# Optimization experiments

Hardware: AMD Instinct MI355X
Metric: run time of the kernel (lower is better)

Reference implementation:

```python
import jax, jax.numpy as jnp
import numpy as np

B, S, HID = 1, 2048, 4096
NH, NKV, D = 32, 8, 128
SCALE = D ** -0.5


def _rope_tables(seq_len, head_dim, base=10000.0):
    inv_freq = 1.0 / (base ** (jnp.arange(0, head_dim, 2, dtype=jnp.float32) / head_dim))
    freqs = jnp.arange(seq_len, dtype=jnp.float32)[:, None] * inv_freq[None, :]  # [S, D/2]
    emb = jnp.concatenate([freqs, freqs], axis=-1)  # [S, D]
    return jnp.cos(emb), jnp.sin(emb)


def _rotate_half(x):
    half = x.shape[-1] // 2
    return jnp.concatenate([-x[..., half:], x[..., :half]], axis=-1)


def setup_inputs() -> dict:
    key = jax.random.key(0)
    ks = jax.random.split(key, 5)
    hidden = jax.random.normal(ks[0], (B, S, HID), dtype=jnp.float32)
    cos, sin = _rope_tables(S, D)
    # additive causal mask: 0 on/below diagonal, large negative above
    neg = jnp.full((S, S), -1e9, dtype=jnp.float32)
    causal_mask = jnp.triu(neg, k=1)[None, None]  # [1,1,S,S]
    std_in = HID ** -0.5
    Wq = jax.random.normal(ks[1], (HID, NH * D), dtype=jnp.float32) * std_in
    Wk = jax.random.normal(ks[2], (HID, NKV * D), dtype=jnp.float32) * std_in
    Wv = jax.random.normal(ks[3], (HID, NKV * D), dtype=jnp.float32) * std_in
    Wo = jax.random.normal(ks[4], (NH * D, HID), dtype=jnp.float32) * ((NH * D) ** -0.5)
    return {"hidden": hidden, "cos": cos, "sin": sin, "causal_mask": causal_mask,
            "Wq": Wq, "Wk": Wk, "Wv": Wv, "Wo": Wo}


def reference(hidden, cos, sin, causal_mask, Wq, Wk, Wv, Wo):
    b, s, _ = hidden.shape
    q = (hidden @ Wq).reshape(b, s, NH, D).transpose(0, 2, 1, 3)    # [B,H,S,D]
    k = (hidden @ Wk).reshape(b, s, NKV, D).transpose(0, 2, 1, 3)   # [B,Hkv,S,D]
    v = (hidden @ Wv).reshape(b, s, NKV, D).transpose(0, 2, 1, 3)
    c = cos[None, None]  # [1,1,S,D]
    sn = sin[None, None]
    q = q * c + _rotate_half(q) * sn
    k = k * c + _rotate_half(k) * sn
    group = NH // NKV
    if group > 1:
        k = jnp.repeat(k, group, axis=1)  # [B,H,S,D]
        v = jnp.repeat(v, group, axis=1)
    scores = jnp.einsum('bhsd,bhtd->bhst', q, k) * SCALE + causal_mask
    attn = jax.nn.softmax(scores.astype(jnp.float32), axis=-1).astype(v.dtype)
    ctx = jnp.einsum('bhst,bhtd->bhsd', attn, v)
    ctx = ctx.transpose(0, 2, 1, 3).reshape(b, s, NH * D)
    return ctx @ Wo
```

## Files before the change

### kernel.cpp

```cpp
#include <hip/hip_runtime.h>
#include <hip/hip_bf16.h>
#include <cstdint>
#include <cstddef>

typedef __attribute__((ext_vector_type(8))) short bf16x8;
typedef __attribute__((ext_vector_type(4))) float f32x4;
typedef __attribute__((ext_vector_type(16))) float f32x16;
typedef __attribute__((ext_vector_type(4))) unsigned int u32x4;

__device__ __forceinline__ unsigned short f2bf(float f) {
  __hip_bfloat16 h = __float2bfloat16(f);
  return *reinterpret_cast<unsigned short*>(&h);
}
__device__ __forceinline__ float bf2f(unsigned short u) {
  __hip_bfloat16 h = *reinterpret_cast<__hip_bfloat16*>(&u);
  return __bfloat162float(h);
}

typedef const __attribute__((address_space(1))) void gas_void;
typedef __attribute__((address_space(3))) void las_void;
__device__ __forceinline__ void gload_lds16(const void* g, void* l) {
  __builtin_amdgcn_global_load_lds((gas_void*)g, (las_void*)l, 16, 0, 0);
}

template <int N>
__device__ __forceinline__ void waitcnt_vm() {
  asm volatile("s_waitcnt vmcnt(%0)" :: "i"(N) : "memory");
}

#define S_LEN 2048
#define HID 4096
#define NH 32
#define NKV 8
#define HD 128
#define NQKV 6144
static const float ATT_SCALE = 0.08838834764831845f;


__global__ void prep_kernel(const float* __restrict__ hidden, short* __restrict__ hid_bf,
                            const float* __restrict__ Wq, const float* __restrict__ Wk,
                            const float* __restrict__ Wv, const float* __restrict__ Wo,
                            short* __restrict__ Wcat, short* __restrict__ WoT) {
  __shared__ float tile[64][33];
  const int bid = blockIdx.x;
  const int t = threadIdx.x;
  if (bid >= 20480) {
    int i = ((bid - 20480) * 256 + t) * 8;
    f32x4 a = *(const f32x4*)(hidden + i);
    f32x4 b = *(const f32x4*)(hidden + i + 4);
    unsigned short o[8];
#pragma unroll
    for (int k = 0; k < 4; ++k) { o[k] = f2bf(a[k]); o[4 + k] = f2bf(b[k]); }
    *(u32x4*)(hid_bf + i) = *(const u32x4*)o;
    return;
  }
  const float* src; short* dst; int N, loc;
  if (bid < 8192)       { src = Wq; dst = Wcat;                      N = 4096; loc = bid; }
  else if (bid < 10240) { src = Wk; dst = Wcat + (size_t)4096 * HID; N = 1024; loc = bid - 8192; }
  else if (bid < 12288) { src = Wv; dst = Wcat + (size_t)5120 * HID; N = 1024; loc = bid - 10240; }
  else                  { src = Wo; dst = WoT;                       N = 4096; loc = bid - 12288; }
  const int kb = (loc & 63) * 64, nb = (loc >> 6) * 32;
  {
    int kr = t >> 3, c4 = (t & 7) * 4;
#pragma unroll
    for (int i = 0; i < 2; ++i) {
      int k = kr + i * 32;
      f32x4 v = *(const f32x4*)(src + (size_t)(kb + k) * N + nb + c4);
      tile[k][c4] = v[0]; tile[k][c4 + 1] = v[1];
      tile[k][c4 + 2] = v[2]; tile[k][c4 + 3] = v[3];
    }
  }
  __syncthreads();
  int n = t >> 3, k0 = (t & 7) * 8;
  unsigned short o[8];
#pragma unroll
  for (int i = 0; i < 8; ++i) o[i] = f2bf(tile[k0 + i][n]);
  *(u32x4*)(dst + (size_t)(nb + n) * HID + kb + k0) = *(const u32x4*)o;
}


template <int MODE, int BM, int BN, int WM, int WN>
__global__ __launch_bounds__(WM * WN * 64, 2) void gemm32_kernel(
    const short* __restrict__ A, const short* __restrict__ Bt,
    int M, int N, int K,
    float* __restrict__ Cf, short* __restrict__ qb_,
    short* __restrict__ kb_, short* __restrict__ vb_) {
  constexpr int NT = WM * WN * 64;
  constexpr int MT = BM / (WM * 32);
  constexpr int NTL = BN / (WN * 32);
  constexpr int LA = (BM / 2) * 8 / NT;
  constexpr int LB = (BN / 2) * 8 / NT;
  constexpr int BUF = (BM + BN) * 64;

  __shared__ short lds[2 * BUF];

  const int tid = threadIdx.x, wid = tid >> 6, lane = tid & 63;
  const int wr = wid / WN, wc = wid % WN;
  const int l31 = lane & 31, lh = lane >> 5;
  const int brow = blockIdx.y * BM, bcol = blockIdx.x * BN;
  const int T = K >> 6;

  f32x16 acc[MT][NTL] = {};

  auto stage_rgn = [&](int kt, int rgn) {
    short* buf = lds + (kt & 1) * BUF;
    if (rgn == 0 || rgn == 3) {
      const int mh = (rgn == 3);
      short* dst = buf + mh * (BM / 2) * 64;
      const short* src = A + (size_t)(brow + mh * (BM / 2)) * K + kt * 64;
#pragma unroll
      for (int i = 0; i < LA; ++i) {
        int slot = i * NT + tid;
        int row = slot >> 3, c2 = slot & 7;
        gload_lds16(src + (size_t)row * K + ((c2 ^ (row & 7)) * 8), dst + slot * 8);
      }
    } else {
      const int nh = (rgn == 2);
      short* dst = buf + BM * 64 + nh * (BN / 2) * 64;
      const short* src = Bt + (size_t)(bcol + nh * (BN / 2)) * K + kt * 64;
#pragma unroll
      for (int i = 0; i < LB; ++i) {
        int slot = i * NT + tid;
        int row = slot >> 3, c2 = slot & 7;
        gload_lds16(src + (size_t)row * K + ((c2 ^ (row & 7)) * 8), dst + slot * 8);
      }
    }
  };

  stage_rgn(0, 0); stage_rgn(0, 1); stage_rgn(0, 2); stage_rgn(0, 3);

  for (int kt = 0; kt < T; ++kt) {
    const bool nl = (kt + 1 < T);
    waitcnt_vm<0>();
    __builtin_amdgcn_s_barrier();
    __builtin_amdgcn_sched_barrier(0);
    if (nl) { stage_rgn(kt + 1, 0); stage_rgn(kt + 1, 1);
              stage_rgn(kt + 1, 2); stage_rgn(kt + 1, 3); }

    const short* As_ = lds + (kt & 1) * BUF;
    const short* Bs_ = As_ + BM * 64;
#pragma unroll
    for (int st = 0; st < 4; ++st) {
      bf16x8 af[MT], bf[NTL];
      const int c = st * 2 + lh;
#pragma unroll
      for (int mt = 0; mt < MT; ++mt) {
        int row = wr * (BM / WM) + mt * 32 + l31;
        af[mt] = *(const bf16x8*)(As_ + row * 64 + ((c ^ (row & 7)) * 8));
      }
#pragma unroll
      for (int nt = 0; nt < NTL; ++nt) {
        int row = wc * (BN / WN) + nt * 32 + l31;
        bf[nt] = *(const bf16x8*)(Bs_ + row * 64 + ((c ^ (row & 7)) * 8));
      }
      __builtin_amdgcn_s_setprio(1);
#pragma unroll
      for (int mt = 0; mt < MT; ++mt)
#pragma unroll
        for (int nt = 0; nt < NTL; ++nt)
          acc[mt][nt] = __builtin_amdgcn_mfma_f32_32x32x16_bf16(
              af[mt], bf[nt], acc[mt][nt], 0, 0, 0);
      __builtin_amdgcn_s_setprio(0);
    }
  }

  if (MODE == 0) {
#pragma unroll
    for (int mt = 0; mt < MT; ++mt)
#pragma unroll
      for (int nt = 0; nt < NTL; ++nt)
#pragma unroll
        for (int reg = 0; reg < 16; ++reg) {
          int row = brow + wr * (BM / WM) + mt * 32 + (reg & 3) + 8 * (reg >> 2) + 4 * lh;
          int col = bcol + wc * (BN / WN) + nt * 32 + l31;
          Cf[(size_t)row * N + col] = acc[mt][nt][reg];
        }
  } else {
#pragma unroll
    for (int nt = 0; nt < NTL; ++nt) {
      const int cb = bcol + wc * (BN / WN) + nt * 32;
      const int d = (cb & 127) + l31;
      if (cb < 4096) {
        unsigned short* dst = (unsigned short*)qb_ + (size_t)(cb >> 7) * S_LEN * HD;
#pragma unroll
        for (int mt = 0; mt < MT; ++mt)
#pragma unroll
          for (int reg = 0; reg < 16; ++reg) {
            int row = brow + wr * (BM / WM) + mt * 32 + (reg & 3) + 8 * (reg >> 2) + 4 * lh;
            dst[(size_t)row * HD + d] = f2bf(acc[mt][nt][reg]);
          }
      } else if (cb < 5120) {
        char* base = (char*)kb_ + ((size_t)((cb - 4096) >> 7) << 19);
#pragma unroll
        for (int mt = 0; mt < MT; ++mt)
#pragma unroll
          for (int reg = 0; reg < 16; ++reg) {
            int row = brow + wr * (BM / WM) + mt * 32 + (reg & 3) + 8 * (reg >> 2) + 4 * lh;
            int krow = row & 63;
            size_t off = ((size_t)(row >> 6) << 14) +
                         ((((krow << 8) + ((d >> 3) << 4)) ^ ((krow & 7) << 4)) + ((d & 7) << 1));
            *(unsigned short*)(base + off) = f2bf(acc[mt][nt][reg]);
          }
      } else {
        char* base = (char*)vb_ + ((size_t)((cb - 5120) >> 7) << 19);
#pragma unroll
        for (int mt = 0; mt < MT; ++mt)
#pragma unroll
          for (int reg = 0; reg < 16; ++reg) {
            int row = brow + wr * (BM / WM) + mt * 32 + (reg & 3) + 8 * (reg >> 2) + 4 * lh;
            int sl = row & 63;
            size_t off = ((size_t)(row >> 6) << 14) +
                         ((((d << 7) + ((sl >> 3) << 4)) ^ ((d & 7) << 4)) + ((sl & 7) << 1));
            *(unsigned short*)(base + off) = f2bf(acc[mt][nt][reg]);
          }
      }
    }
  }
}

__global__ void rope_kernel(short* __restrict__ qbuf, short* __restrict__ kbuf,
                            const float* __restrict__ cosT, const float* __restrict__ sinT) {
  int idx = blockIdx.x * 256 + threadIdx.x;
  const int total = (NH + NKV) * S_LEN * 64;
  if (idx >= total) return;
  int d = idx & 63;
  int rowi = idx >> 6;
  int s;
  unsigned short *p1, *p2;
  if (rowi < NH * S_LEN) {
    unsigned short* base = (unsigned short*)qbuf + (size_t)rowi * HD;
    s = rowi & (S_LEN - 1);
    p1 = base + d; p2 = base + d + 64;
  } else {
    int kr = rowi - NH * S_LEN;
    int kvh = kr >> 11; s = kr & (S_LEN - 1);
    char* base = (char*)kbuf + ((size_t)kvh << 19) + ((size_t)(s >> 6) << 14);
    int krow = s & 63, swz = (krow & 7) << 4;
    int dd = d + 64;
    p1 = (unsigned short*)(base + ((((krow << 8) + ((d >> 3) << 4)) ^ swz) + ((d & 7) << 1)));
    p2 = (unsigned short*)(base + ((((krow << 8) + ((dd >> 3) << 4)) ^ swz) + ((dd & 7) << 1)));
  }
  float x1 = bf2f(*p1);
  float x2 = bf2f(*p2);
  float c1 = cosT[s * HD + d], s1 = sinT[s * HD + d];
  *p1 = f2bf(x1 * c1 - x2 * s1);
  *p2 = f2bf(x2 * c1 + x1 * s1);
}

__global__ __launch_bounds__(512, 2) void attn_kernel(const short* __restrict__ qb_,
                                                      const short* __restrict__ kb_,
                                                      const short* __restrict__ vb_,
                                                      short* __restrict__ ctx) {
  const int bid = blockIdx.x;
  const int kvh = bid & 7;
  const int idx = bid >> 3;
  const int h = kvh * 4 + (idx & 3);
  const int slot = idx >> 2;
  const int tid = threadIdx.x, wid = tid >> 6, lane = tid & 63;
  const int r = lane & 15, g = lane >> 4;

  __shared__ short Ks[2][64 * 128];
  __shared__ short Vts[2][128 * 64];
  __shared__ short Ps[8][16 * 64];

  const int qb2s[2] = { slot, 15 - slot };
  const int nt0 = 2 * qb2s[0] + 2;
  const int T = 34;

  const char* kvbase_k = (const char*)kb_ + ((size_t)kvh << 19);
  const char* kvbase_v = (const char*)vb_ + ((size_t)kvh << 19);

  auto stage = [&](int tg, int b) {
    int kvt = (tg < nt0) ? tg : (tg - nt0);
    const char* kt = kvbase_k + ((size_t)kvt << 14);
    const char* vt = kvbase_v + ((size_t)kvt << 14);
#pragma unroll
    for (int i = 0; i < 2; ++i) {
      int ch = i * 8 + wid;
      gload_lds16(kt + ch * 1024 + lane * 16, (char*)&Ks[b][0] + ch * 1024);
      gload_lds16(vt + ch * 1024 + lane * 16, (char*)&Vts[b][0] + ch * 1024);
    }
  };

  stage(0, 0);
  int cur = 0, tglob = 0;

  for (int sec = 0; sec < 2; ++sec) {
    const int qb2 = qb2s[sec];
    const int nt = 2 * qb2 + 2;
    const int rowbase = qb2 * 128 + wid * 16;

    const unsigned short* qptr =
        (const unsigned short*)qb_ + ((size_t)h * S_LEN + rowbase) * HD;
    bf16x8 qf[4];
#pragma unroll
    for (int s4 = 0; s4 < 4; ++s4)
      qf[s4] = *(const bf16x8*)(qptr + (size_t)r * HD + s4 * 32 + g * 8);

    f32x4 oacc[8] = {};
    float m_run[4], l_run[4];
#pragma unroll
    for (int j = 0; j < 4; ++j) { m_run[j] = -1e30f; l_run[j] = 0.f; }

    for (int kvt = 0; kvt < nt; ++kvt, ++tglob) {
      __syncthreads();
      if (tglob + 1 < T) stage(tglob + 1, cur ^ 1);

      const char* Kc = (const char*)&Ks[cur][0];
      const char* Vc = (const char*)&Vts[cur][0];

      f32x4 sv[4] = {};
      __builtin_amdgcn_s_setprio(1);
#pragma unroll
      for (int n = 0; n < 4; ++n) {
        int krow = n * 16 + r;
        int swz = (krow & 7) << 4;
#pragma unroll
        for (int s4 = 0; s4 < 4; ++s4) {
          bf16x8 kf = *(const bf16x8*)(Kc + ((krow * 256 + s4 * 64 + g * 16) ^ swz));
          sv[n] = __builtin_amdgcn_mfma_f32_16x16x32_bf16(qf[s4], kf, sv[n], 0, 0, 0);
        }
      }
      __builtin_amdgcn_s_setprio(0);

      if (kvt * 64 + 63 > rowbase) {
#pragma unroll
        for (int n = 0; n < 4; ++n)
#pragma unroll
          for (int j = 0; j < 4; ++j) {
            int colg = kvt * 64 + n * 16 + r;
            int rowg = rowbase + g * 4 + j;
            sv[n][j] = (colg <= rowg) ? sv[n][j] * ATT_SCALE : -1e30f;
          }
      } else {
#pragma unroll
        for (int n = 0; n < 4; ++n)
#pragma unroll
          for (int j = 0; j < 4; ++j) sv[n][j] *= ATT_SCALE;
      }

      float pmax[4];
#pragma unroll
      for (int j = 0; j < 4; ++j)
        pmax[j] = fmaxf(fmaxf(sv[0][j], sv[1][j]), fmaxf(sv[2][j], sv[3][j]));
#pragma unroll
      for (int msk = 1; msk <= 8; msk <<= 1)
#pragma unroll
        for (int j = 0; j < 4; ++j) pmax[j] = fmaxf(pmax[j], __shfl_xor(pmax[j], msk));

      float sf[4], rsum[4];
#pragma unroll
      for (int j = 0; j < 4; ++j) {
        float mn = fmaxf(m_run[j], pmax[j]);
        sf[j] = __expf(m_run[j] - mn);
        m_run[j] = mn;
        rsum[j] = 0.f;
      }
#pragma unroll
      for (int n = 0; n < 4; ++n)
#pragma unroll
        for (int j = 0; j < 4; ++j) {
          float p = __expf(sv[n][j] - m_run[j]);
          sv[n][j] = p;
          rsum[j] += p;
        }
#pragma unroll
      for (int msk = 1; msk <= 8; msk <<= 1)
#pragma unroll
        for (int j = 0; j < 4; ++j) rsum[j] += __shfl_xor(rsum[j], msk);
#pragma unroll
      for (int j = 0; j < 4; ++j) l_run[j] = l_run[j] * sf[j] + rsum[j];
#pragma unroll
      for (int t = 0; t < 8; ++t)
#pragma unroll
        for (int j = 0; j < 4; ++j) oacc[t][j] *= sf[j];

#pragma unroll
      for (int n = 0; n < 4; ++n)
#pragma unroll
        for (int j = 0; j < 4; ++j) {
          int prow = g * 4 + j, pcol = n * 16 + r;
          int poff = (prow * 128 + pcol * 2) ^ ((prow & 7) << 4);
          *(unsigned short*)((char*)&Ps[wid][0] + poff) = f2bf(sv[n][j]);
        }

      __builtin_amdgcn_s_setprio(1);
#pragma unroll
      for (int s4 = 0; s4 < 2; ++s4) {
        bf16x8 pf = *(const bf16x8*)((const char*)&Ps[wid][0] +
                                     ((r * 128 + s4 * 64 + g * 16) ^ ((r & 7) << 4)));
#pragma unroll
        for (int t = 0; t < 8; ++t) {
          int vrow = t * 16 + r;
          bf16x8 vf = *(const bf16x8*)(Vc + ((vrow * 128 + s4 * 64 + g * 16) ^ ((vrow & 7) << 4)));
          oacc[t] = __builtin_amdgcn_mfma_f32_16x16x32_bf16(pf, vf, oacc[t], 0, 0, 0);
        }
      }
      __builtin_amdgcn_s_setprio(0);
      cur ^= 1;
    }

    float inv[4];
#pragma unroll
    for (int j = 0; j < 4; ++j) inv[j] = 1.0f / l_run[j];
#pragma unroll
    for (int t = 0; t < 8; ++t)
#pragma unroll
      for (int j = 0; j < 4; ++j) {
        int rowg = rowbase + g * 4 + j;
        int colg = h * HD + t * 16 + r;
        ((unsigned short*)ctx)[(size_t)rowg * HID + colg] = f2bf(oacc[t][j] * inv[j]);
      }
  }
}

extern "C" void kernel_launch(void* const* d_in, const int* in_sizes, int n_in,
                              void* d_out, int out_size, void* d_ws, size_t ws_size,
                              hipStream_t stream) {
  const float* hidden = (const float*)d_in[0];
  const float* cosT   = (const float*)d_in[1];
  const float* sinT   = (const float*)d_in[2];
  const float* Wq = (const float*)d_in[4];
  const float* Wk = (const float*)d_in[5];
  const float* Wv = (const float*)d_in[6];
  const float* Wo = (const float*)d_in[7];
  float* out = (float*)d_out;

  char* ws = (char*)d_ws;
  short* hid_bf = (short*)(ws);
  short* Wcat   = (short*)(ws + 16777216);
  short* WoT    = (short*)(ws + 67108864);
  short* qbuf   = (short*)(ws + 100663296);
  short* kbuf   = (short*)(ws + 117440512);
  short* vbuf   = (short*)(ws + 121634816);
  short* ctx    = (short*)(ws + 125829120);

  prep_kernel<<<24576, 256, 0, stream>>>(hidden, hid_bf, Wq, Wk, Wv, Wo, Wcat, WoT);

  gemm32_kernel<1, 128, 384, 2, 4><<<dim3(16, 16), 512, 0, stream>>>(
      hid_bf, Wcat, S_LEN, NQKV, HID, nullptr, qbuf, kbuf, vbuf);

  rope_kernel<<<20480, 256, 0, stream>>>(qbuf, kbuf, cosT, sinT);

  attn_kernel<<<256, 512, 0, stream>>>(qbuf, kbuf, vbuf, ctx);

  gemm32_kernel<0, 128, 256, 2, 4><<<dim3(16, 16), 512, 0, stream>>>(
      ctx, WoT, S_LEN, HID, HID, out, nullptr, nullptr, nullptr);
}
```

Baseline: 338.8 us.

## Pre-tile GEMM operands into contiguous block layout for linear LDS staging

The prep kernel and the attention epilogue now write hidden, the concatenated QKV weights, Wo^T and ctx in a tiled layout. Each 64-wide k-slice of a 128-row (or BN-row) block becomes one contiguous chunk, grouped by 8-element column. The GEMM then stages each tile with fully linear 16-byte global-to-LDS loads and reads fragments without XOR swizzle arithmetic. This is meant to make the global loads perfectly coalesced and cut address math. The trade-offs are that the hidden conversion becomes a transpose through shared memory, ctx is written with scattered 2-byte stores, and the LDS reads lose their bank-conflict swizzle.

Result: faster. 327.5 us (-3.3%).

```diff
diff --git a/kernel.cpp b/kernel.cpp
--- a/kernel.cpp
+++ b/kernel.cpp
@@ -44,21 +44,35 @@
   __shared__ float tile[64][33];
   const int bid = blockIdx.x;
   const int t = threadIdx.x;
+
   if (bid >= 20480) {
-    int i = ((bid - 20480) * 256 + t) * 8;
-    f32x4 a = *(const f32x4*)(hidden + i);
-    f32x4 b = *(const f32x4*)(hidden + i + 4);
+    const int hbid = bid - 20480;
+    const int kb = (hbid & 63) * 64, sb = (hbid >> 6) * 32;
+    {
+      int sr = t >> 3, k4 = (t & 7) * 4;
+#pragma unroll
+      for (int i = 0; i < 2; ++i) {
+        f32x4 v = *(const f32x4*)(hidden + (size_t)(sb + sr) * HID + kb + i * 32 + k4);
+#pragma unroll
+        for (int jj = 0; jj < 4; ++jj) tile[i * 32 + k4 + jj][sr] = v[jj];
+      }
+    }
+    __syncthreads();
+    const int ts = t & 31, c = t >> 5;
+    const int s = sb + ts;
     unsigned short o[8];
 #pragma unroll
-    for (int k = 0; k < 4; ++k) { o[k] = f2bf(a[k]); o[4 + k] = f2bf(b[k]); }
-    *(u32x4*)(hid_bf + i) = *(const u32x4*)o;
+    for (int i = 0; i < 8; ++i) o[i] = f2bf(tile[c * 8 + i][ts]);
+    size_t off16 = (((size_t)(s >> 7) * 64 + (kb >> 6)) * 8 + c) * 128 + (s & 127);
+    *(u32x4*)(hid_bf + off16 * 8) = *(const u32x4*)o;
     return;
   }
-  const float* src; short* dst; int N, loc;
-  if (bid < 8192)       { src = Wq; dst = Wcat;                      N = 4096; loc = bid; }
-  else if (bid < 10240) { src = Wk; dst = Wcat + (size_t)4096 * HID; N = 1024; loc = bid - 8192; }
-  else if (bid < 12288) { src = Wv; dst = Wcat + (size_t)5120 * HID; N = 1024; loc = bid - 10240; }
-  else                  { src = Wo; dst = WoT;                       N = 4096; loc = bid - 12288; }
+
+  const float* src; short* dst; int N, loc, noff, BNp;
+  if (bid < 8192)       { src = Wq; dst = Wcat; N = 4096; loc = bid;         noff = 0;    BNp = 384; }
+  else if (bid < 10240) { src = Wk; dst = Wcat; N = 1024; loc = bid - 8192;  noff = 4096; BNp = 384; }
+  else if (bid < 12288) { src = Wv; dst = Wcat; N = 1024; loc = bid - 10240; noff = 5120; BNp = 384; }
+  else                  { src = Wo; dst = WoT;  N = 4096; loc = bid - 12288; noff = 0;    BNp = 256; }
   const int kb = (loc & 63) * 64, nb = (loc >> 6) * 32;
   {
     int kr = t >> 3, c4 = (t & 7) * 4;
@@ -71,26 +85,30 @@
     }
   }
   __syncthreads();
-  int n = t >> 3, k0 = (t & 7) * 8;
+  const int tn = t & 31, c = t >> 5;
+  const int n = noff + nb + tn;
+  const int nblk = n / BNp, nrow = n % BNp;
   unsigned short o[8];
 #pragma unroll
-  for (int i = 0; i < 8; ++i) o[i] = f2bf(tile[k0 + i][n]);
-  *(u32x4*)(dst + (size_t)(nb + n) * HID + kb + k0) = *(const u32x4*)o;
-}
-
-
-template <int MODE, int BM, int BN, int WM, int WN>
-__global__ __launch_bounds__(WM * WN * 64, 2) void gemm32_kernel(
+  for (int i = 0; i < 8; ++i) o[i] = f2bf(tile[c * 8 + i][tn]);
+  size_t off16 = (((size_t)nblk * 64 + (kb >> 6)) * 8 + c) * BNp + nrow;
+  *(u32x4*)(dst + off16 * 8) = *(const u32x4*)o;
+}
+
+template <int MODE, int BN>
+__global__ __launch_bounds__(512, 2) void gemm32t_kernel(
     const short* __restrict__ A, const short* __restrict__ Bt,
-    int M, int N, int K,
+    int N, int K,
     float* __restrict__ Cf, short* __restrict__ qb_,
     short* __restrict__ kb_, short* __restrict__ vb_) {
-  constexpr int NT = WM * WN * 64;
+  constexpr int BM = 128, WM = 2, WN = 4;
   constexpr int MT = BM / (WM * 32);
   constexpr int NTL = BN / (WN * 32);
-  constexpr int LA = (BM / 2) * 8 / NT;
-  constexpr int LB = (BN / 2) * 8 / NT;
-  constexpr int BUF = (BM + BN) * 64;
+  constexpr int ASZ = 8 * BM * 8;
+  constexpr int BSZ = 8 * BN * 8;
+  constexpr int LA = ASZ / (512 * 8);
+  constexpr int LB = BSZ / (512 * 8);
+  constexpr int BUF = ASZ + BSZ;
 
   __shared__ short lds[2 * BUF];
 
@@ -102,57 +120,44 @@
 
   f32x16 acc[MT][NTL] = {};
 
-  auto stage_rgn = [&](int kt, int rgn) {
-    short* buf = lds + (kt & 1) * BUF;
-    if (rgn == 0 || rgn == 3) {
-      const int mh = (rgn == 3);
-      short* dst = buf + mh * (BM / 2) * 64;
-      const short* src = A + (size_t)(brow + mh * (BM / 2)) * K + kt * 64;
-#pragma unroll
-      for (int i = 0; i < LA; ++i) {
-        int slot = i * NT + tid;
-        int row = slot >> 3, c2 = slot & 7;
-        gload_lds16(src + (size_t)row * K + ((c2 ^ (row & 7)) * 8), dst + slot * 8);
-      }
-    } else {
-      const int nh = (rgn == 2);
-      short* dst = buf + BM * 64 + nh * (BN / 2) * 64;
-      const short* src = Bt + (size_t)(bcol + nh * (BN / 2)) * K + kt * 64;
-#pragma unroll
-      for (int i = 0; i < LB; ++i) {
-        int slot = i * NT + tid;
-        int row = slot >> 3, c2 = slot & 7;
-        gload_lds16(src + (size_t)row * K + ((c2 ^ (row & 7)) * 8), dst + slot * 8);
-      }
+  auto stage = [&](int kt) {
+    short* dstA = lds + (kt & 1) * BUF;
+    const short* srcA = A + (size_t)(blockIdx.y * 64 + kt) * ASZ;
+#pragma unroll
+    for (int i = 0; i < LA; ++i) {
+      int slot = i * 512 + tid;
+      gload_lds16(srcA + slot * 8, dstA + slot * 8);
+    }
+    short* dstB = dstA + ASZ;
+    const short* srcB = Bt + (size_t)(blockIdx.x * 64 + kt) * BSZ;
+#pragma unroll
+    for (int i = 0; i < LB; ++i) {
+      int slot = i * 512 + tid;
+      gload_lds16(srcB + slot * 8, dstB + slot * 8);
     }
   };
 
-  stage_rgn(0, 0); stage_rgn(0, 1); stage_rgn(0, 2); stage_rgn(0, 3);
+  stage(0);
 
   for (int kt = 0; kt < T; ++kt) {
     const bool nl = (kt + 1 < T);
     waitcnt_vm<0>();
     __builtin_amdgcn_s_barrier();
     __builtin_amdgcn_sched_barrier(0);
-    if (nl) { stage_rgn(kt + 1, 0); stage_rgn(kt + 1, 1);
-              stage_rgn(kt + 1, 2); stage_rgn(kt + 1, 3); }
+    if (nl) stage(kt + 1);
 
     const short* As_ = lds + (kt & 1) * BUF;
-    const short* Bs_ = As_ + BM * 64;
+    const short* Bs_ = As_ + ASZ;
 #pragma unroll
     for (int st = 0; st < 4; ++st) {
       bf16x8 af[MT], bf[NTL];
       const int c = st * 2 + lh;
 #pragma unroll
-      for (int mt = 0; mt < MT; ++mt) {
-        int row = wr * (BM / WM) + mt * 32 + l31;
-        af[mt] = *(const bf16x8*)(As_ + row * 64 + ((c ^ (row & 7)) * 8));
-      }
-#pragma unroll
-      for (int nt = 0; nt < NTL; ++nt) {
-        int row = wc * (BN / WN) + nt * 32 + l31;
-        bf[nt] = *(const bf16x8*)(Bs_ + row * 64 + ((c ^ (row & 7)) * 8));
-      }
+      for (int mt = 0; mt < MT; ++mt)
+        af[mt] = *(const bf16x8*)(As_ + (c * BM + wr * 64 + mt * 32 + l31) * 8);
+#pragma unroll
+      for (int nt = 0; nt < NTL; ++nt)
+        bf[nt] = *(const bf16x8*)(Bs_ + (c * BN + wc * (BN / WN) + nt * 32 + l31) * 8);
       __builtin_amdgcn_s_setprio(1);
 #pragma unroll
       for (int mt = 0; mt < MT; ++mt)
@@ -171,7 +176,7 @@
       for (int nt = 0; nt < NTL; ++nt)
 #pragma unroll
         for (int reg = 0; reg < 16; ++reg) {
-          int row = brow + wr * (BM / WM) + mt * 32 + (reg & 3) + 8 * (reg >> 2) + 4 * lh;
+          int row = brow + wr * 64 + mt * 32 + (reg & 3) + 8 * (reg >> 2) + 4 * lh;
           int col = bcol + wc * (BN / WN) + nt * 32 + l31;
           Cf[(size_t)row * N + col] = acc[mt][nt][reg];
         }
@@ -186,7 +191,7 @@
         for (int mt = 0; mt < MT; ++mt)
 #pragma unroll
           for (int reg = 0; reg < 16; ++reg) {
-            int row = brow + wr * (BM / WM) + mt * 32 + (reg & 3) + 8 * (reg >> 2) + 4 * lh;
+            int row = brow + wr * 64 + mt * 32 + (reg & 3) + 8 * (reg >> 2) + 4 * lh;
             dst[(size_t)row * HD + d] = f2bf(acc[mt][nt][reg]);
           }
       } else if (cb < 5120) {
@@ -195,7 +200,7 @@
         for (int mt = 0; mt < MT; ++mt)
 #pragma unroll
           for (int reg = 0; reg < 16; ++reg) {
-            int row = brow + wr * (BM / WM) + mt * 32 + (reg & 3) + 8 * (reg >> 2) + 4 * lh;
+            int row = brow + wr * 64 + mt * 32 + (reg & 3) + 8 * (reg >> 2) + 4 * lh;
             int krow = row & 63;
             size_t off = ((size_t)(row >> 6) << 14) +
                          ((((krow << 8) + ((d >> 3) << 4)) ^ ((krow & 7) << 4)) + ((d & 7) << 1));
@@ -207,7 +212,7 @@
         for (int mt = 0; mt < MT; ++mt)
 #pragma unroll
           for (int reg = 0; reg < 16; ++reg) {
-            int row = brow + wr * (BM / WM) + mt * 32 + (reg & 3) + 8 * (reg >> 2) + 4 * lh;
+            int row = brow + wr * 64 + mt * 32 + (reg & 3) + 8 * (reg >> 2) + 4 * lh;
             int sl = row & 63;
             size_t off = ((size_t)(row >> 6) << 14) +
                          ((((d << 7) + ((sl >> 3) << 4)) ^ ((d & 7) << 4)) + ((sl & 7) << 1));
@@ -407,9 +412,10 @@
     for (int t = 0; t < 8; ++t)
 #pragma unroll
       for (int j = 0; j < 4; ++j) {
-        int rowg = rowbase + g * 4 + j;
+        int s = rowbase + g * 4 + j;
         int colg = h * HD + t * 16 + r;
-        ((unsigned short*)ctx)[(size_t)rowg * HID + colg] = f2bf(oacc[t][j] * inv[j]);
+        size_t off16 = (((size_t)(s >> 7) * 64 + (colg >> 6)) * 8 + ((colg >> 3) & 7)) * 128 + (s & 127);
+        *(unsigned short*)((char*)ctx + off16 * 16 + (colg & 7) * 2) = f2bf(oacc[t][j] * inv[j]);
       }
   }
 }
@@ -437,13 +443,13 @@
 
   prep_kernel<<<24576, 256, 0, stream>>>(hidden, hid_bf, Wq, Wk, Wv, Wo, Wcat, WoT);
 
-  gemm32_kernel<1, 128, 384, 2, 4><<<dim3(16, 16), 512, 0, stream>>>(
-      hid_bf, Wcat, S_LEN, NQKV, HID, nullptr, qbuf, kbuf, vbuf);
+  gemm32t_kernel<1, 384><<<dim3(16, 16), 512, 0, stream>>>(
+      hid_bf, Wcat, NQKV, HID, nullptr, qbuf, kbuf, vbuf);
 
   rope_kernel<<<20480, 256, 0, stream>>>(qbuf, kbuf, cosT, sinT);
 
   attn_kernel<<<256, 512, 0, stream>>>(qbuf, kbuf, vbuf, ctx);
 
-  gemm32_kernel<0, 128, 256, 2, 4><<<dim3(16, 16), 512, 0, stream>>>(
-      ctx, WoT, S_LEN, HID, HID, out, nullptr, nullptr, nullptr);
-}
+  gemm32t_kernel<0, 256><<<dim3(16, 16), 512, 0, stream>>>(
+      ctx, WoT, HID, HID, out, nullptr, nullptr, nullptr);
+}
```
